# Performance work log

Measured on AMD Instinct MI355X. Metric: run time of the kernel, lower is better.

The kernel has to match this reference:

```python
import jax, jax.numpy as jnp
import numpy as np

B, T, D = 8, 8192, 512
H, P = 4, 24
HD = D // H
TEMP = 0.07
TOPK = max(1, int(P * 0.5))  # 12
LN_EPS = 1e-5
NORM_EPS = 1e-12


def setup_inputs() -> dict:
    key = jax.random.key(0)
    ks = jax.random.split(key, 12)
    s = 0.02
    return {
        "x": jax.random.normal(ks[0], (B, T, D), dtype=jnp.float32),
        "proto": jax.random.normal(ks[1], (P, D), dtype=jnp.float32) * s,
        "ln_g": jnp.ones((D,), dtype=jnp.float32),
        "ln_b": jnp.zeros((D,), dtype=jnp.float32),
        "Wq": jax.random.normal(ks[2], (D, D), dtype=jnp.float32) * s,
        "Wk": jax.random.normal(ks[3], (D, D), dtype=jnp.float32) * s,
        "Wv": jax.random.normal(ks[4], (D, D), dtype=jnp.float32) * s,
        "W1": jax.random.normal(ks[5], (D, D), dtype=jnp.float32) * s,
        "b1": jnp.zeros((D,), dtype=jnp.float32),
        "W2": jax.random.normal(ks[6], (D, D), dtype=jnp.float32) * s,
        "b2": jnp.zeros((D,), dtype=jnp.float32),
    }


def _l2norm(t):
    n = jnp.sqrt(jnp.sum(t * t, axis=-1, keepdims=True))
    return t / jnp.maximum(n, NORM_EPS)


def reference(x, proto, ln_g, ln_b, Wq, Wk, Wv, W1, b1, W2, b2):
    # pre-LayerNorm over last dim
    mu = jnp.mean(x, axis=-1, keepdims=True)
    var = jnp.mean((x - mu) ** 2, axis=-1, keepdims=True)
    xn = (x - mu) / jnp.sqrt(var + LN_EPS) * ln_g + ln_b

    K = xn @ Wk.T                      # [B,T,D]
    V = xn @ Wv.T                      # [B,T,D]
    Qp = proto @ Wq.T                  # [P,D] (shared across batch)

    Qh = _l2norm(Qp.reshape(P, H, HD).transpose(1, 0, 2))          # [H,P,hd]
    Kh = _l2norm(K.reshape(B, T, H, HD).transpose(0, 2, 1, 3))      # [B,H,T,hd]
    Vh = V.reshape(B, T, H, HD).transpose(0, 2, 1, 3)               # [B,H,T,hd]

    scores = jnp.einsum('hpd,bhtd->bhpt', Qh, Kh) / TEMP            # [B,H,P,T]
    attn = jnp.nan_to_num(jax.nn.softmax(scores, axis=-1), nan=0.0)
    proto_tokens = jnp.einsum('bhpt,bhtd->bhpd', attn, Vh)          # [B,H,P,hd]
    proto_tokens = proto_tokens.transpose(0, 2, 1, 3).reshape(B, P, D)

    proto_scores = jnp.sum(proto_tokens ** 2, axis=2)               # [B,P]
    _, idx = jax.lax.top_k(proto_scores, TOPK)                      # [B,topk]
    topk_tokens = jnp.take_along_axis(proto_tokens, idx[:, :, None], axis=1)
    z = jnp.mean(topk_tokens, axis=1)                               # [B,D]

    h = jax.nn.silu(z @ W1.T + b1)
    return h @ W2.T + b2
```

## Files before the change

kernel.cpp:

```cpp
#include <hip/hip_runtime.h>
#include <hip/hip_bf16.h>

#define BB 8
#define TSEQ 8192
#define DDIM 512
#define NH 4
#define HDIM 128
#define NP 24
#define NPAD 32
#define NTOPK 12
#define NCHUNK 32
#define TCHUNK 256
#define NTILES 8

typedef _Float16 half8_t __attribute__((ext_vector_type(8)));
typedef _Float16 half4_t __attribute__((ext_vector_type(4)));
typedef _Float16 half2_t __attribute__((ext_vector_type(2)));
typedef float f32x4_t __attribute__((ext_vector_type(4)));

#define MFMA(a, b, c) __builtin_amdgcn_mfma_f32_16x16x32_f16((a), (b), (c), 0, 0, 0)

#define WGBAR() do { asm volatile("s_waitcnt lgkmcnt(0)" ::: "memory"); \
                     __builtin_amdgcn_s_barrier(); } while (0)


__global__ __launch_bounds__(256) void qh_kernel(
    const float* __restrict__ proto, const float* __restrict__ Wq, float* __restrict__ qhs)
{
  const int p = blockIdx.x, tid = threadIdx.x;
  __shared__ float prow[DDIM];
  __shared__ float qp[DDIM];
  __shared__ float np[NH][8];
  __shared__ float nb[NH];
  prow[tid] = proto[(size_t)p * DDIM + tid];
  prow[tid + 256] = proto[(size_t)p * DDIM + tid + 256];
  __syncthreads();
#pragma unroll
  for (int i = 0; i < 2; ++i) {
    int dd = tid + i * 256;
    const float4* w4 = reinterpret_cast<const float4*>(Wq + (size_t)dd * DDIM);
    const float4* p4 = reinterpret_cast<const float4*>(prow);
    float s = 0.f;
    for (int d = 0; d < 128; ++d) {
      float4 av = p4[d], bv = w4[d];
      s += av.x * bv.x + av.y * bv.y + av.z * bv.z + av.w * bv.w;
    }
    qp[dd] = s;
  }
  __syncthreads();
  {
    int hh = tid >> 3, pr = tid & 7;
    if (hh < NH) {
      float s = 0.f;
      for (int k = 0; k < 16; ++k) { float v = qp[hh * HDIM + pr * 16 + k]; s += v * v; }
      np[hh][pr] = s;
    }
  }
  __syncthreads();
  if (tid < NH) {
    float s = 0.f;
    for (int k = 0; k < 8; ++k) s += np[tid][k];
    nb[tid] = 1.f / (fmaxf(sqrtf(s), 1e-12f) * 0.07f);
  }
  __syncthreads();
#pragma unroll
  for (int i = 0; i < 2; ++i) {
    int dd = tid + i * 256;
    int hh = dd >> 7, jj = dd & 127;
    qhs[((size_t)hh * NP + p) * HDIM + jj] = qp[dd] * nb[hh];
  }
}

__global__ __launch_bounds__(256) void wg16_kernel(
    const float* __restrict__ Wk, const float* __restrict__ ln_g, const float* __restrict__ ln_b,
    _Float16* __restrict__ wg16, float* __restrict__ uvK, float* __restrict__ vvK)
{
  const int j = blockIdx.x, tid = threadIdx.x;
  __shared__ float su[256], sv[256];
  float w0 = Wk[(size_t)j * 512 + tid], w1 = Wk[(size_t)j * 512 + tid + 256];
  float g0 = ln_g[tid], g1 = ln_g[tid + 256];
  float b0 = ln_b[tid], b1 = ln_b[tid + 256];
  wg16[(size_t)j * 512 + tid] = (_Float16)(w0 * g0);
  wg16[(size_t)j * 512 + tid + 256] = (_Float16)(w1 * g1);
  su[tid] = w0 * g0 + w1 * g1;
  sv[tid] = w0 * b0 + w1 * b1;
  __syncthreads();
  for (int s = 128; s > 0; s >>= 1) {
    if (tid < s) { su[tid] += su[tid + s]; sv[tid] += sv[tid + s]; }
    __syncthreads();
  }
  if (tid == 0) { uvK[j] = su[0]; vvK[j] = sv[0]; }
}

__global__ __launch_bounds__(256) void wqkg_kernel(
    const float* __restrict__ qhs, const float* __restrict__ Wk,
    const float* __restrict__ ln_g, const float* __restrict__ ln_b,
    _Float16* __restrict__ wqkg16, float* __restrict__ uq, float* __restrict__ vq)
{
  const int blk = blockIdx.x, tid = threadIdx.x;
  const int p = blk & 31, h = blk >> 5;
  __shared__ float su[256], sv[256];
  if (p >= NP) {
    wqkg16[((size_t)(h * 32 + p)) * 512 + tid] = (_Float16)0.f;
    wqkg16[((size_t)(h * 32 + p)) * 512 + tid + 256] = (_Float16)0.f;
    if (tid == 0) { uq[h * 32 + p] = 0.f; vq[h * 32 + p] = 0.f; }
    return;
  }
  __shared__ float qv[HDIM];
  if (tid < HDIM) qv[tid] = qhs[((size_t)h * NP + p) * HDIM + tid];
  __syncthreads();
  float s0 = 0.f, s1 = 0.f;
  for (int j = 0; j < HDIM; ++j) {
    float q = qv[j];
    const float* wr = Wk + (size_t)(h * 128 + j) * 512;
    s0 += q * wr[tid];
    s1 += q * wr[tid + 256];
  }
  float g0 = ln_g[tid], g1 = ln_g[tid + 256];
  float b0 = ln_b[tid], b1 = ln_b[tid + 256];
  wqkg16[((size_t)(h * 32 + p)) * 512 + tid] = (_Float16)(s0 * g0);
  wqkg16[((size_t)(h * 32 + p)) * 512 + tid + 256] = (_Float16)(s1 * g1);
  su[tid] = s0 * g0 + s1 * g1;
  sv[tid] = s0 * b0 + s1 * b1;
  __syncthreads();
  for (int s = 128; s > 0; s >>= 1) {
    if (tid < s) { su[tid] += su[tid + s]; sv[tid] += sv[tid + s]; }
    __syncthreads();
  }
  if (tid == 0) { uq[h * 32 + p] = su[0]; vq[h * 32 + p] = sv[0]; }
}

__global__ __launch_bounds__(512, 1) void knorm6(
    const float* __restrict__ x, const _Float16* __restrict__ wg16,
    const float* __restrict__ uvK, const float* __restrict__ vvK,
    float* __restrict__ normINV, float* __restrict__ miv)
{
  const int tid = threadIdx.x;
  const int w = tid >> 6, l = tid & 63;
  const int g = l >> 4, a = l & 15;
  const int blk = blockIdx.x;
  const int tc = blk & 31, g2 = (blk >> 5) & 1, b = blk >> 6;
  const int ct0 = tc * 256;

  __shared__ __align__(16) unsigned char xs_raw[32 * 1040];
  __shared__ float normp_s[8][32];
  __shared__ float2 miv_s[32];

  const int jrow0 = g2 * 256 + 32 * w + a;
  half8_t wgf[2][16];
#pragma unroll
  for (int kst = 0; kst < 16; ++kst) {
    wgf[0][kst] = *reinterpret_cast<const half8_t*>(wg16 + (size_t)jrow0 * 512 + kst * 32 + g * 8);
    wgf[1][kst] = *reinterpret_cast<const half8_t*>(wg16 + (size_t)(jrow0 + 16) * 512 + kst * 32 + g * 8);
  }
  const float u0 = uvK[jrow0], u1 = uvK[jrow0 + 16];
  const float v0 = vvK[jrow0], v1 = vvK[jrow0 + 16];

  const float4* xc4 = reinterpret_cast<const float4*>(x) + ((size_t)(b * TSEQ + ct0)) * 128;

  float4 praw[4][2];
#pragma unroll
  for (int tt = 0; tt < 4; ++tt)
#pragma unroll
    for (int i = 0; i < 2; ++i)
      praw[tt][i] = xc4[(size_t)(4 * w + tt) * 128 + l + 64 * i];

  for (int tile = 0; tile < NTILES; ++tile) {
    float sA[4], sB[4];
#pragma unroll
    for (int tt = 0; tt < 4; ++tt) {
      float4 v0f = praw[tt][0], v1f = praw[tt][1];
      sA[tt] = (v0f.x + v0f.y) + (v0f.z + v0f.w) + (v1f.x + v1f.y) + (v1f.z + v1f.w);
      sB[tt] = (v0f.x * v0f.x + v0f.y * v0f.y) + (v0f.z * v0f.z + v0f.w * v0f.w)
             + (v1f.x * v1f.x + v1f.y * v1f.y) + (v1f.z * v1f.z + v1f.w * v1f.w);
    }
#pragma unroll
    for (int m = 1; m < 64; m <<= 1)
#pragma unroll
      for (int tt = 0; tt < 4; ++tt) { sA[tt] += __shfl_xor(sA[tt], m); sB[tt] += __shfl_xor(sB[tt], m); }
    float muv[4], ivv[4];
#pragma unroll
    for (int tt = 0; tt < 4; ++tt) {
      float mu = sA[tt] * (1.f / 512.f);
      float var = sB[tt] * (1.f / 512.f) - mu * mu;
      muv[tt] = mu; ivv[tt] = rsqrtf(var + 1e-5f);
    }

    WGBAR();

#pragma unroll
    for (int tt = 0; tt < 4; ++tt)
#pragma unroll
      for (int i = 0; i < 2; ++i) {
        float4 v = praw[tt][i];
        half4_t hx;
        hx[0] = (_Float16)v.x; hx[1] = (_Float16)v.y; hx[2] = (_Float16)v.z; hx[3] = (_Float16)v.w;
        *reinterpret_cast<half4_t*>(xs_raw + (4 * w + tt) * 1040 + 8 * l + 512 * i) = hx;
      }
#pragma unroll
    for (int tt = 0; tt < 4; ++tt) {
      if (l == tt) {
        miv_s[4 * w + tt] = make_float2(muv[tt], ivv[tt]);
        if (g2 == 0) {
          size_t t = (size_t)b * TSEQ + ct0 + tile * 32 + 4 * w + tt;
          miv[2 * t] = muv[tt];
          miv[2 * t + 1] = ivv[tt];
        }
      }
    }
    if (tile + 1 < NTILES) {
#pragma unroll
      for (int tt = 0; tt < 4; ++tt)
#pragma unroll
        for (int i = 0; i < 2; ++i)
          praw[tt][i] = xc4[(size_t)((tile + 1) * 32 + 4 * w + tt) * 128 + l + 64 * i];
    }
    WGBAR();

    f32x4_t kacc[2][2];
    const f32x4_t vzero = {0.f, 0.f, 0.f, 0.f};
    kacc[0][0] = vzero; kacc[0][1] = vzero; kacc[1][0] = vzero; kacc[1][1] = vzero;
#pragma unroll
    for (int kst = 0; kst < 16; ++kst) {
#pragma unroll
      for (int mt = 0; mt < 2; ++mt) {
        half8_t af = *reinterpret_cast<const half8_t*>(xs_raw + (16 * mt + a) * 1040 + kst * 64 + g * 16);
        kacc[mt][0] = MFMA(af, wgf[0][kst], kacc[mt][0]);
        kacc[mt][1] = MFMA(af, wgf[1][kst], kacc[mt][1]);
      }
    }
    float np2[2][4];
#pragma unroll
    for (int mt = 0; mt < 2; ++mt)
#pragma unroll
      for (int r = 0; r < 4; ++r) {
        float2 mvt = miv_s[16 * mt + 4 * g + r];
        float k0 = mvt.y * (kacc[mt][0][r] - mvt.x * u0) + v0;
        float k1 = mvt.y * (kacc[mt][1][r] - mvt.x * u1) + v1;
        np2[mt][r] = k0 * k0 + k1 * k1;
      }
#pragma unroll
    for (int m = 1; m < 16; m <<= 1)
#pragma unroll
      for (int mt = 0; mt < 2; ++mt)
#pragma unroll
        for (int r = 0; r < 4; ++r) np2[mt][r] += __shfl_xor(np2[mt][r], m);
    if (a == 0) {
#pragma unroll
      for (int mt = 0; mt < 2; ++mt)
#pragma unroll
        for (int r = 0; r < 4; ++r) normp_s[w][16 * mt + 4 * g + r] = np2[mt][r];
    }
    WGBAR();
    if (tid < 64) {
      const int t = tid & 31, hl = tid >> 5;
      float s = normp_s[hl * 4 + 0][t] + normp_s[hl * 4 + 1][t]
              + normp_s[hl * 4 + 2][t] + normp_s[hl * 4 + 3][t];
      normINV[((size_t)b * NH + 2 * g2 + hl) * TSEQ + ct0 + tile * 32 + t] =
          rsqrtf(fmaxf(s, 1e-24f));
    }
  }
}

__global__ __launch_bounds__(512, 1) void attn6(
    const float* __restrict__ x, const _Float16* __restrict__ wqkg16,
    const float* __restrict__ normINV, const float* __restrict__ miv,
    const float* __restrict__ uq, const float* __restrict__ vq,
    const float* __restrict__ ln_g, const float* __restrict__ ln_b,
    float* __restrict__ ml, _Float16* __restrict__ xbar)
{
  const int tid = threadIdx.x;
  const int w = tid >> 6, l = tid & 63;
  const int g = l >> 4, a = l & 15;
  const int blk = blockIdx.x;
  const int c = blk & 31, g2 = (blk >> 5) & 1, b = blk >> 6;

  __shared__ __align__(16) unsigned char xs_raw[32 * 1040];
  __shared__ __align__(16) unsigned char xt_raw[512 * 72];
  __shared__ __align__(16) unsigned char wl_raw[64 * 80];
  __shared__ float mArr_s[64], lArr_s[64], fbuf_s[64], c1Arr_s[64];

  if (tid < 64) { mArr_s[tid] = -1e30f; lArr_s[tid] = 0.f; c1Arr_s[tid] = 0.f; }

  f32x4_t acc3[4][4];
  const f32x4_t vzero = {0.f, 0.f, 0.f, 0.f};
#pragma unroll
  for (int mA = 0; mA < 4; ++mA)
#pragma unroll
    for (int nt = 0; nt < 4; ++nt) acc3[mA][nt] = vzero;

  const float4* xc4 = reinterpret_cast<const float4*>(x) + ((size_t)(b * TSEQ + c * TCHUNK)) * 128;
  const _Float16* wqbase = wqkg16 + ((size_t)(g2 * 64 + 16 * w + a)) * 512 + g * 8;
  const float* nbase0 = normINV + ((size_t)b * NH + 2 * g2 + (w >> 1)) * TSEQ + c * TCHUNK;
  const float* mivc = miv + 2 * ((size_t)b * TSEQ + c * TCHUNK);
  float uqp = 0.f, vqp = 0.f;
  if (w < 4) { uqp = uq[g2 * 64 + 16 * w + a]; vqp = vq[g2 * 64 + 16 * w + a]; }

  float4 praw[4][2];
#pragma unroll
  for (int tt = 0; tt < 4; ++tt)
#pragma unroll
    for (int i = 0; i < 2; ++i)
      praw[tt][i] = xc4[(size_t)(4 * w + tt) * 128 + l + 64 * i];

  for (int tile = 0; tile < NTILES; ++tile) {
    WGBAR();

#pragma unroll
    for (int tt = 0; tt < 4; ++tt)
#pragma unroll
      for (int i = 0; i < 2; ++i) {
        float4 v = praw[tt][i];
        half4_t hx;
        hx[0] = (_Float16)v.x; hx[1] = (_Float16)v.y; hx[2] = (_Float16)v.z; hx[3] = (_Float16)v.w;
        *reinterpret_cast<half4_t*>(xs_raw + (4 * w + tt) * 1040 + 8 * l + 512 * i) = hx;
      }
    {
      const float* pf = reinterpret_cast<const float*>(praw);
#pragma unroll
      for (int i = 0; i < 2; ++i)
#pragma unroll
        for (int e = 0; e < 4; ++e) {
          half4_t hv;
          hv[0] = (_Float16)pf[0 * 8 + i * 4 + e];
          hv[1] = (_Float16)pf[1 * 8 + i * 4 + e];
          hv[2] = (_Float16)pf[2 * 8 + i * 4 + e];
          hv[3] = (_Float16)pf[3 * 8 + i * 4 + e];
          int d = 4 * l + 256 * i + e;
          *reinterpret_cast<half4_t*>(xt_raw + d * 72 + 8 * (w ^ ((d >> 4) & 7))) = hv;
        }
    }
    if (tile + 1 < NTILES) {
#pragma unroll
      for (int tt = 0; tt < 4; ++tt)
#pragma unroll
        for (int i = 0; i < 2; ++i)
          praw[tt][i] = xc4[(size_t)((tile + 1) * 32 + 4 * w + tt) * 128 + l + 64 * i];
    }
    f32x4_t niv4[2];
    f32x4_t mv[2][2];
    if (w < 4) {
      const float* nb2 = nbase0 + tile * 32 + 4 * g;
      niv4[0] = *reinterpret_cast<const f32x4_t*>(nb2);
      niv4[1] = *reinterpret_cast<const f32x4_t*>(nb2 + 16);
#pragma unroll
      for (int mt = 0; mt < 2; ++mt) {
        const float* mb = mivc + 2 * (tile * 32 + 16 * mt + 4 * g);
        mv[mt][0] = *reinterpret_cast<const f32x4_t*>(mb);
        mv[mt][1] = *reinterpret_cast<const f32x4_t*>(mb + 4);
      }
    }
    WGBAR();

    if (w < 4) {
      f32x4_t qacc[2] = {vzero, vzero};
#pragma unroll
      for (int kst = 0; kst < 16; ++kst) {
        half8_t bq8 = *reinterpret_cast<const half8_t*>(wqbase + kst * 32);
#pragma unroll
        for (int mt = 0; mt < 2; ++mt) {
          half8_t af = *reinterpret_cast<const half8_t*>(xs_raw + (16 * mt + a) * 1040 + kst * 64 + g * 16);
          qacc[mt] = MFMA(af, bq8, qacc[mt]);
        }
      }
      const int p = 16 * w + a;
      float sc[2][4], ivr[2][4], imr[2][4];
      float cmax = -3e38f;
#pragma unroll
      for (int mt = 0; mt < 2; ++mt)
#pragma unroll
        for (int r = 0; r < 4; ++r) {
          float mu = mv[mt][r >> 1][2 * (r & 1)];
          float iv = mv[mt][r >> 1][2 * (r & 1) + 1];
          ivr[mt][r] = iv;
          imr[mt][r] = iv * mu;
          float s = (iv * (qacc[mt][r] - mu * uqp) + vqp) * niv4[mt][r];
          sc[mt][r] = s;
          cmax = fmaxf(cmax, s);
        }
      cmax = fmaxf(cmax, __shfl_xor(cmax, 16));
      cmax = fmaxf(cmax, __shfl_xor(cmax, 32));
      float mo = mArr_s[p];
      float mn = fmaxf(mo, cmax);
      float fe = __expf(mo - mn);
      float ls = 0.f, ls1 = 0.f;
#pragma unroll
      for (int mt = 0; mt < 2; ++mt) {
        half4_t wp;
#pragma unroll
        for (int r = 0; r < 4; ++r) {
          float e = __expf(sc[mt][r] - mn);
          ls += e;
          ls1 += e * imr[mt][r];
          wp[r] = (_Float16)(e * ivr[mt][r]);
        }
        *reinterpret_cast<half4_t*>(wl_raw + p * 80 + 32 * mt + 8 * g) = wp;
      }
      ls += __shfl_xor(ls, 16);   ls += __shfl_xor(ls, 32);
      ls1 += __shfl_xor(ls1, 16); ls1 += __shfl_xor(ls1, 32);
      if (l < 16) {
        mArr_s[p] = mn;
        lArr_s[p] = lArr_s[p] * fe + ls;
        c1Arr_s[p] = c1Arr_s[p] * fe + ls1;
        fbuf_s[p] = fe;
      }
    }
    WGBAR();

#pragma unroll
    for (int mA = 0; mA < 4; ++mA)
#pragma unroll
      for (int r = 0; r < 4; ++r) {
        float f = fbuf_s[16 * mA + 4 * g + r];
#pragma unroll
        for (int nt = 0; nt < 4; ++nt) acc3[mA][nt][r] *= f;
      }
    {
      half8_t wlf[4];
#pragma unroll
      for (int mA = 0; mA < 4; ++mA)
        wlf[mA] = *reinterpret_cast<const half8_t*>(wl_raw + (16 * mA + a) * 80 + 16 * g);
#pragma unroll
      for (int nt = 0; nt < 4; ++nt) {
        const int d = 64 * w + 16 * nt + a;
        const unsigned char* rowp = xt_raw + d * 72;
        const int key = (d >> 4) & 7;
        half4_t lo = *reinterpret_cast<const half4_t*>(rowp + 8 * ((2 * g) ^ key));
        half4_t hi = *reinterpret_cast<const half4_t*>(rowp + 8 * ((2 * g + 1) ^ key));
        half8_t bf;
        bf[0] = lo[0]; bf[1] = lo[1]; bf[2] = lo[2]; bf[3] = lo[3];
        bf[4] = hi[0]; bf[5] = hi[1]; bf[6] = hi[2]; bf[7] = hi[3];
#pragma unroll
        for (int mA = 0; mA < 4; ++mA) acc3[mA][nt] = MFMA(wlf[mA], bf, acc3[mA][nt]);
      }
    }
  }

  __syncthreads();
  float gd[4], bd[4];
#pragma unroll
  for (int nt = 0; nt < 4; ++nt) {
    gd[nt] = ln_g[64 * w + 16 * nt + a];
    bd[nt] = ln_b[64 * w + 16 * nt + a];
  }
#pragma unroll
  for (int mA = 0; mA < 4; ++mA)
#pragma unroll
    for (int r = 0; r < 4; ++r) {
      const int p = 16 * mA + 4 * g + r;
      const float c1p = c1Arr_s[p], lp = lArr_s[p];
      const int h = 2 * g2 + (p >> 5), ph = p & 31;
      _Float16* xb = xbar + ((((size_t)b * NH + h) * NCHUNK + c) * NPAD + ph) * DDIM;
#pragma unroll
      for (int nt = 0; nt < 4; ++nt)
        xb[64 * w + 16 * nt + a] = (_Float16)(gd[nt] * (acc3[mA][nt][r] - c1p) + bd[nt] * lp);
    }
  if (tid < 64) {
    const int h = 2 * g2 + (tid >> 5), ph = tid & 31;
    size_t mlb = ((((size_t)b * NH + h) * NCHUNK + c) * NPAD + ph) * 2;
    ml[mlb] = mArr_s[tid];
    ml[mlb + 1] = lArr_s[tid];
  }
}

__global__ __launch_bounds__(256) void reduce_proto(
    const float* __restrict__ ml, const _Float16* __restrict__ xbar,
    const float* __restrict__ Wv, float* __restrict__ proto_t)
{
  const int tid = threadIdx.x;
  const int blk = blockIdx.x;
  const int p = blk % NP;
  const int h = (blk / NP) % NH;
  const int b = blk / (NP * NH);
  const int wv = tid >> 6, ln = tid & 63;

  __shared__ float fch[NCHUNK];
  __shared__ float LinvS;
  __shared__ __align__(16) float xbs[DDIM];

  if (tid < NCHUNK) {
    size_t idx = ((((size_t)b * NH + h) * NCHUNK + tid) * NPAD + p) * 2;
    float m = ml[idx], lv = ml[idx + 1];
    float mstar = m;
#pragma unroll
    for (int k = 16; k >= 1; k >>= 1) mstar = fmaxf(mstar, __shfl_xor(mstar, k));
    float f = __expf(m - mstar);
    float Lp = lv * f;
#pragma unroll
    for (int k = 16; k >= 1; k >>= 1) Lp += __shfl_xor(Lp, k);
    fch[tid] = f;
    if (tid == 0) LinvS = 1.f / fmaxf(Lp, 1e-30f);
  }
  __syncthreads();
  float a0 = 0.f, a1 = 0.f;
  for (int cc = 0; cc < NCHUNK; ++cc) {
    float f = fch[cc];
    const _Float16* src = xbar + ((((size_t)b * NH + h) * NCHUNK + cc) * NPAD + p) * DDIM;
    half2_t v = *reinterpret_cast<const half2_t*>(src + 2 * tid);
    a0 += f * (float)v[0];
    a1 += f * (float)v[1];
  }
  xbs[2 * tid] = a0;
  xbs[2 * tid + 1] = a1;
  __syncthreads();
  const float Linv = LinvS;
  const float4* zp = reinterpret_cast<const float4*>(xbs);
  const float4 z0 = zp[2 * ln], z1 = zp[2 * ln + 1];
#pragma unroll 4
  for (int j0 = 0; j0 < 32; ++j0) {
    const int j = wv * 32 + j0;
    const float4* wrow = reinterpret_cast<const float4*>(Wv + (size_t)(h * HDIM + j) * DDIM);
    float4 w0 = wrow[2 * ln], w1 = wrow[2 * ln + 1];
    float s = w0.x * z0.x + w0.y * z0.y + w0.z * z0.z + w0.w * z0.w
            + w1.x * z1.x + w1.y * z1.y + w1.z * z1.z + w1.w * z1.w;
#pragma unroll
    for (int m = 1; m < 64; m <<= 1) s += __shfl_xor(s, m);
    if (ln == 0)
      proto_t[((size_t)b * NP + p) * DDIM + h * HDIM + j] = s * Linv;
  }
}

__global__ __launch_bounds__(256) void topk_mean(
    const float* __restrict__ proto_t, float* __restrict__ zbuf)
{
  const int b = blockIdx.x, tid = threadIdx.x;
  __shared__ float pt[NP][DDIM];
  __shared__ float spart[NP][8];
  __shared__ float sc[NP];
  __shared__ int sel[NP];
  for (int i = tid; i < NP * DDIM; i += 256) pt[i >> 9][i & 511] = proto_t[(size_t)b * NP * DDIM + i];
  __syncthreads();
  {
    int p = tid >> 3, pr = tid & 7;
    if (p < NP) {
      float s = 0.f;
      for (int k = 0; k < 64; ++k) { float v = pt[p][pr * 64 + k]; s += v * v; }
      spart[p][pr] = s;
    }
  }
  __syncthreads();
  if (tid < NP) {
    float s = 0.f;
    for (int k = 0; k < 8; ++k) s += spart[tid][k];
    sc[tid] = s;
  }
  __syncthreads();
  if (tid < NP) {
    float sv = sc[tid]; int rank = 0;
    for (int q = 0; q < NP; ++q) { float so = sc[q]; if (so > sv || (so == sv && q < tid)) ++rank; }
    sel[tid] = (rank < NTOPK) ? 1 : 0;
  }
  __syncthreads();
#pragma unroll
  for (int i = 0; i < 2; ++i) {
    const int d = tid + i * 256;
    float z0 = 0.f;
#pragma unroll
    for (int p = 0; p < NP; ++p)
      if (sel[p]) z0 += pt[p][d];
    zbuf[(size_t)b * DDIM + d] = z0 * (1.f / NTOPK);
  }
}

template <int ACT>
__global__ __launch_bounds__(256) void mlp_fc(
    const float* __restrict__ zin, const float* __restrict__ W,
    const float* __restrict__ bias, float* __restrict__ outp)
{
  const int tid = threadIdx.x;
  const int wv = tid >> 6, ln = tid & 63;
  const int j = blockIdx.x * 4 + wv;
  __shared__ __align__(16) float zs[BB][DDIM];
  for (int i = tid; i < BB * DDIM; i += 256) zs[i >> 9][i & 511] = zin[i];
  __syncthreads();
  const float4* wrow = reinterpret_cast<const float4*>(W + (size_t)j * DDIM);
  const float4 w0 = wrow[2 * ln], w1 = wrow[2 * ln + 1];
  const float bj = bias[j];
#pragma unroll
  for (int b = 0; b < BB; ++b) {
    const float4* zp = reinterpret_cast<const float4*>(zs[b]);
    float4 z0 = zp[2 * ln], z1 = zp[2 * ln + 1];
    float s = w0.x * z0.x + w0.y * z0.y + w0.z * z0.z + w0.w * z0.w
            + w1.x * z1.x + w1.y * z1.y + w1.z * z1.z + w1.w * z1.w;
#pragma unroll
    for (int m = 1; m < 64; m <<= 1) s += __shfl_xor(s, m);
    if (ln == b) {
      s += bj;
      if (ACT) s = s / (1.f + expf(-s));
      outp[(size_t)b * DDIM + j] = s;
    }
  }
}

extern "C" void kernel_launch(void* const* d_in, const int* in_sizes, int n_in,
                              void* d_out, int out_size, void* d_ws, size_t ws_size,
                              hipStream_t stream)
{
  const float* x    = (const float*)d_in[0];
  const float* prt  = (const float*)d_in[1];
  const float* ln_g = (const float*)d_in[2];
  const float* ln_b = (const float*)d_in[3];
  const float* Wq   = (const float*)d_in[4];
  const float* Wk   = (const float*)d_in[5];
  const float* Wv   = (const float*)d_in[6];
  const float* W1   = (const float*)d_in[7];
  const float* b1   = (const float*)d_in[8];
  const float* W2   = (const float*)d_in[9];
  const float* b2   = (const float*)d_in[10];
  float* out = (float*)d_out;
  float* ws = (float*)d_ws;

  float* qhs = ws;
  float* ml  = ws + 12288;
  _Float16* xb16 = (_Float16*)(ws + 77824);
  float* pt  = ws + 8466432;
  _Float16* wg16   = (_Float16*)(ws + 8564736);
  _Float16* wqkg16 = (_Float16*)(ws + 8695808);
  float* normINV = ws + 8728576;
  float* miv     = ws + 8990720;
  float* uvK     = ws + 9121792;
  float* vvK     = ws + 9122304;
  float* uq      = ws + 9122816;
  float* vq      = ws + 9122944;
  float* zbuf    = ws + 9123072;
  float* hbuf    = ws + 9127168;

  qh_kernel<<<NP, 256, 0, stream>>>(prt, Wq, qhs);
  wg16_kernel<<<512, 256, 0, stream>>>(Wk, ln_g, ln_b, wg16, uvK, vvK);
  wqkg_kernel<<<128, 256, 0, stream>>>(qhs, Wk, ln_g, ln_b, wqkg16, uq, vq);
  knorm6<<<BB * 2 * 32, 512, 0, stream>>>(x, wg16, uvK, vvK, normINV, miv);
  attn6<<<BB * 2 * NCHUNK, 512, 0, stream>>>(x, wqkg16, normINV, miv, uq, vq, ln_g, ln_b, ml, xb16);
  reduce_proto<<<BB * NH * NP, 256, 0, stream>>>(ml, xb16, Wv, pt);
  topk_mean<<<BB, 256, 0, stream>>>(pt, zbuf);
  mlp_fc<1><<<128, 256, 0, stream>>>(zbuf, W1, b1, hbuf);
  mlp_fc<0><<<128, 256, 0, stream>>>(hbuf, W2, b2, out);
}
```

Before: 241.4 us.

## Fuse key-norm computation into attention kernel using idle warps

```diff
diff --git a/kernel.cpp b/kernel.cpp
--- a/kernel.cpp
+++ b/kernel.cpp
@@ -130,33 +130,49 @@
   if (tid == 0) { uq[h * 32 + p] = su[0]; vq[h * 32 + p] = sv[0]; }
 }
 
-__global__ __launch_bounds__(512, 1) void knorm6(
+__global__ __launch_bounds__(512, 1) void attn7(
     const float* __restrict__ x, const _Float16* __restrict__ wg16,
+    const _Float16* __restrict__ wqkg16,
     const float* __restrict__ uvK, const float* __restrict__ vvK,
-    float* __restrict__ normINV, float* __restrict__ miv)
+    const float* __restrict__ uq, const float* __restrict__ vq,
+    const float* __restrict__ ln_g, const float* __restrict__ ln_b,
+    float* __restrict__ ml, _Float16* __restrict__ xbar)
 {
   const int tid = threadIdx.x;
   const int w = tid >> 6, l = tid & 63;
   const int g = l >> 4, a = l & 15;
   const int blk = blockIdx.x;
-  const int tc = blk & 31, g2 = (blk >> 5) & 1, b = blk >> 6;
-  const int ct0 = tc * 256;
+  const int c = blk & 31, g2 = (blk >> 5) & 1, b = blk >> 6;
 
   __shared__ __align__(16) unsigned char xs_raw[32 * 1040];
-  __shared__ float normp_s[8][32];
+  __shared__ __align__(16) unsigned char xt_raw[512 * 72];
+  __shared__ __align__(16) unsigned char wl_raw[64 * 80];
+  __shared__ float mArr_s[64], lArr_s[64], fbuf_s[64], c1Arr_s[64];
+  __shared__ float normp_s[4][32];
   __shared__ float2 miv_s[32];
 
-  const int jrow0 = g2 * 256 + 32 * w + a;
-  half8_t wgf[2][16];
-#pragma unroll
-  for (int kst = 0; kst < 16; ++kst) {
-    wgf[0][kst] = *reinterpret_cast<const half8_t*>(wg16 + (size_t)jrow0 * 512 + kst * 32 + g * 8);
-    wgf[1][kst] = *reinterpret_cast<const half8_t*>(wg16 + (size_t)(jrow0 + 16) * 512 + kst * 32 + g * 8);
-  }
-  const float u0 = uvK[jrow0], u1 = uvK[jrow0 + 16];
-  const float v0 = vvK[jrow0], v1 = vvK[jrow0 + 16];
-
-  const float4* xc4 = reinterpret_cast<const float4*>(x) + ((size_t)(b * TSEQ + ct0)) * 128;
+  if (tid < 64) { mArr_s[tid] = -1e30f; lArr_s[tid] = 0.f; c1Arr_s[tid] = 0.f; }
+
+  f32x4_t acc3[4][4];
+  const f32x4_t vzero = {0.f, 0.f, 0.f, 0.f};
+#pragma unroll
+  for (int mA = 0; mA < 4; ++mA)
+#pragma unroll
+    for (int nt = 0; nt < 4; ++nt) acc3[mA][nt] = vzero;
+
+  const float4* xc4 = reinterpret_cast<const float4*>(x) + ((size_t)(b * TSEQ + c * TCHUNK)) * 128;
+  const _Float16* wqbase = wqkg16 + ((size_t)(g2 * 64 + 16 * w + a)) * 512 + g * 8;
+  const int q = w & 3;
+  const int jrow0 = g2 * 256 + 64 * q + a;
+  float uqp = 0.f, vqp = 0.f;
+  float uK[4], vK[4];
+  if (w < 4) {
+    uqp = uq[g2 * 64 + 16 * w + a];
+    vqp = vq[g2 * 64 + 16 * w + a];
+  } else {
+#pragma unroll
+    for (int nt = 0; nt < 4; ++nt) { uK[nt] = uvK[jrow0 + 16 * nt]; vK[nt] = vvK[jrow0 + 16 * nt]; }
+  }
 
   float4 praw[4][2];
 #pragma unroll
@@ -186,124 +202,6 @@
       muv[tt] = mu; ivv[tt] = rsqrtf(var + 1e-5f);
     }
 
-    WGBAR();
-
-#pragma unroll
-    for (int tt = 0; tt < 4; ++tt)
-#pragma unroll
-      for (int i = 0; i < 2; ++i) {
-        float4 v = praw[tt][i];
-        half4_t hx;
-        hx[0] = (_Float16)v.x; hx[1] = (_Float16)v.y; hx[2] = (_Float16)v.z; hx[3] = (_Float16)v.w;
-        *reinterpret_cast<half4_t*>(xs_raw + (4 * w + tt) * 1040 + 8 * l + 512 * i) = hx;
-      }
-#pragma unroll
-    for (int tt = 0; tt < 4; ++tt) {
-      if (l == tt) {
-        miv_s[4 * w + tt] = make_float2(muv[tt], ivv[tt]);
-        if (g2 == 0) {
-          size_t t = (size_t)b * TSEQ + ct0 + tile * 32 + 4 * w + tt;
-          miv[2 * t] = muv[tt];
-          miv[2 * t + 1] = ivv[tt];
-        }
-      }
-    }
-    if (tile + 1 < NTILES) {
-#pragma unroll
-      for (int tt = 0; tt < 4; ++tt)
-#pragma unroll
-        for (int i = 0; i < 2; ++i)
-          praw[tt][i] = xc4[(size_t)((tile + 1) * 32 + 4 * w + tt) * 128 + l + 64 * i];
-    }
-    WGBAR();
-
-    f32x4_t kacc[2][2];
-    const f32x4_t vzero = {0.f, 0.f, 0.f, 0.f};
-    kacc[0][0] = vzero; kacc[0][1] = vzero; kacc[1][0] = vzero; kacc[1][1] = vzero;
-#pragma unroll
-    for (int kst = 0; kst < 16; ++kst) {
-#pragma unroll
-      for (int mt = 0; mt < 2; ++mt) {
-        half8_t af = *reinterpret_cast<const half8_t*>(xs_raw + (16 * mt + a) * 1040 + kst * 64 + g * 16);
-        kacc[mt][0] = MFMA(af, wgf[0][kst], kacc[mt][0]);
-        kacc[mt][1] = MFMA(af, wgf[1][kst], kacc[mt][1]);
-      }
-    }
-    float np2[2][4];
-#pragma unroll
-    for (int mt = 0; mt < 2; ++mt)
-#pragma unroll
-      for (int r = 0; r < 4; ++r) {
-        float2 mvt = miv_s[16 * mt + 4 * g + r];
-        float k0 = mvt.y * (kacc[mt][0][r] - mvt.x * u0) + v0;
-        float k1 = mvt.y * (kacc[mt][1][r] - mvt.x * u1) + v1;
-        np2[mt][r] = k0 * k0 + k1 * k1;
-      }
-#pragma unroll
-    for (int m = 1; m < 16; m <<= 1)
-#pragma unroll
-      for (int mt = 0; mt < 2; ++mt)
-#pragma unroll
-        for (int r = 0; r < 4; ++r) np2[mt][r] += __shfl_xor(np2[mt][r], m);
-    if (a == 0) {
-#pragma unroll
-      for (int mt = 0; mt < 2; ++mt)
-#pragma unroll
-        for (int r = 0; r < 4; ++r) normp_s[w][16 * mt + 4 * g + r] = np2[mt][r];
-    }
-    WGBAR();
-    if (tid < 64) {
-      const int t = tid & 31, hl = tid >> 5;
-      float s = normp_s[hl * 4 + 0][t] + normp_s[hl * 4 + 1][t]
-              + normp_s[hl * 4 + 2][t] + normp_s[hl * 4 + 3][t];
-      normINV[((size_t)b * NH + 2 * g2 + hl) * TSEQ + ct0 + tile * 32 + t] =
-          rsqrtf(fmaxf(s, 1e-24f));
-    }
-  }
-}
-
-__global__ __launch_bounds__(512, 1) void attn6(
-    const float* __restrict__ x, const _Float16* __restrict__ wqkg16,
-    const float* __restrict__ normINV, const float* __restrict__ miv,
-    const float* __restrict__ uq, const float* __restrict__ vq,
-    const float* __restrict__ ln_g, const float* __restrict__ ln_b,
-    float* __restrict__ ml, _Float16* __restrict__ xbar)
-{
-  const int tid = threadIdx.x;
-  const int w = tid >> 6, l = tid & 63;
-  const int g = l >> 4, a = l & 15;
-  const int blk = blockIdx.x;
-  const int c = blk & 31, g2 = (blk >> 5) & 1, b = blk >> 6;
-
-  __shared__ __align__(16) unsigned char xs_raw[32 * 1040];
-  __shared__ __align__(16) unsigned char xt_raw[512 * 72];
-  __shared__ __align__(16) unsigned char wl_raw[64 * 80];
-  __shared__ float mArr_s[64], lArr_s[64], fbuf_s[64], c1Arr_s[64];
-
-  if (tid < 64) { mArr_s[tid] = -1e30f; lArr_s[tid] = 0.f; c1Arr_s[tid] = 0.f; }
-
-  f32x4_t acc3[4][4];
-  const f32x4_t vzero = {0.f, 0.f, 0.f, 0.f};
-#pragma unroll
-  for (int mA = 0; mA < 4; ++mA)
-#pragma unroll
-    for (int nt = 0; nt < 4; ++nt) acc3[mA][nt] = vzero;
-
-  const float4* xc4 = reinterpret_cast<const float4*>(x) + ((size_t)(b * TSEQ + c * TCHUNK)) * 128;
-  const _Float16* wqbase = wqkg16 + ((size_t)(g2 * 64 + 16 * w + a)) * 512 + g * 8;
-  const float* nbase0 = normINV + ((size_t)b * NH + 2 * g2 + (w >> 1)) * TSEQ + c * TCHUNK;
-  const float* mivc = miv + 2 * ((size_t)b * TSEQ + c * TCHUNK);
-  float uqp = 0.f, vqp = 0.f;
-  if (w < 4) { uqp = uq[g2 * 64 + 16 * w + a]; vqp = vq[g2 * 64 + 16 * w + a]; }
-
-  float4 praw[4][2];
-#pragma unroll
-  for (int tt = 0; tt < 4; ++tt)
-#pragma unroll
-    for (int i = 0; i < 2; ++i)
-      praw[tt][i] = xc4[(size_t)(4 * w + tt) * 128 + l + 64 * i];
-
-  for (int tile = 0; tile < NTILES; ++tile) {
     WGBAR();
 
 #pragma unroll
@@ -330,6 +228,9 @@
           *reinterpret_cast<half4_t*>(xt_raw + d * 72 + 8 * (w ^ ((d >> 4) & 7))) = hv;
         }
     }
+#pragma unroll
+    for (int tt = 0; tt < 4; ++tt)
+      if (l == tt) miv_s[4 * w + tt] = make_float2(muv[tt], ivv[tt]);
     if (tile + 1 < NTILES) {
 #pragma unroll
       for (int tt = 0; tt < 4; ++tt)
@@ -337,23 +238,10 @@
         for (int i = 0; i < 2; ++i)
           praw[tt][i] = xc4[(size_t)((tile + 1) * 32 + 4 * w + tt) * 128 + l + 64 * i];
     }
-    f32x4_t niv4[2];
-    f32x4_t mv[2][2];
+    WGBAR();
+
+    f32x4_t qacc[2] = {vzero, vzero};
     if (w < 4) {
-      const float* nb2 = nbase0 + tile * 32 + 4 * g;
-      niv4[0] = *reinterpret_cast<const f32x4_t*>(nb2);
-      niv4[1] = *reinterpret_cast<const f32x4_t*>(nb2 + 16);
-#pragma unroll
-      for (int mt = 0; mt < 2; ++mt) {
-        const float* mb = mivc + 2 * (tile * 32 + 16 * mt + 4 * g);
-        mv[mt][0] = *reinterpret_cast<const f32x4_t*>(mb);
-        mv[mt][1] = *reinterpret_cast<const f32x4_t*>(mb + 4);
-      }
-    }
-    WGBAR();
-
-    if (w < 4) {
-      f32x4_t qacc[2] = {vzero, vzero};
 #pragma unroll
       for (int kst = 0; kst < 16; ++kst) {
         half8_t bq8 = *reinterpret_cast<const half8_t*>(wqbase + kst * 32);
@@ -363,6 +251,57 @@
           qacc[mt] = MFMA(af, bq8, qacc[mt]);
         }
       }
+    } else {
+      f32x4_t kacc[2][4];
+#pragma unroll
+      for (int mt = 0; mt < 2; ++mt)
+#pragma unroll
+        for (int nt = 0; nt < 4; ++nt) kacc[mt][nt] = vzero;
+#pragma unroll
+      for (int kst = 0; kst < 16; ++kst) {
+        half8_t bnt[4];
+#pragma unroll
+        for (int nt = 0; nt < 4; ++nt)
+          bnt[nt] = *reinterpret_cast<const half8_t*>(
+              wg16 + (size_t)(jrow0 + 16 * nt) * 512 + kst * 32 + g * 8);
+#pragma unroll
+        for (int mt = 0; mt < 2; ++mt) {
+          half8_t af = *reinterpret_cast<const half8_t*>(xs_raw + (16 * mt + a) * 1040 + kst * 64 + g * 16);
+#pragma unroll
+          for (int nt = 0; nt < 4; ++nt) kacc[mt][nt] = MFMA(af, bnt[nt], kacc[mt][nt]);
+        }
+      }
+      float np2[2][4];
+#pragma unroll
+      for (int mt = 0; mt < 2; ++mt)
+#pragma unroll
+        for (int r = 0; r < 4; ++r) {
+          float2 mvt = miv_s[16 * mt + 4 * g + r];
+          float s = 0.f;
+#pragma unroll
+          for (int nt = 0; nt < 4; ++nt) {
+            float k = mvt.y * (kacc[mt][nt][r] - mvt.x * uK[nt]) + vK[nt];
+            s += k * k;
+          }
+          np2[mt][r] = s;
+        }
+#pragma unroll
+      for (int m = 1; m < 16; m <<= 1)
+#pragma unroll
+        for (int mt = 0; mt < 2; ++mt)
+#pragma unroll
+          for (int r = 0; r < 4; ++r) np2[mt][r] += __shfl_xor(np2[mt][r], m);
+      if (a == 0) {
+#pragma unroll
+        for (int mt = 0; mt < 2; ++mt)
+#pragma unroll
+          for (int r = 0; r < 4; ++r) normp_s[q][16 * mt + 4 * g + r] = np2[mt][r];
+      }
+    }
+    WGBAR();
+
+    if (w < 4) {
+      const int hl = w >> 1;
       const int p = 16 * w + a;
       float sc[2][4], ivr[2][4], imr[2][4];
       float cmax = -3e38f;
@@ -370,11 +309,13 @@
       for (int mt = 0; mt < 2; ++mt)
 #pragma unroll
         for (int r = 0; r < 4; ++r) {
-          float mu = mv[mt][r >> 1][2 * (r & 1)];
-          float iv = mv[mt][r >> 1][2 * (r & 1) + 1];
-          ivr[mt][r] = iv;
-          imr[mt][r] = iv * mu;
-          float s = (iv * (qacc[mt][r] - mu * uqp) + vqp) * niv4[mt][r];
+          const int t = 16 * mt + 4 * g + r;
+          float2 mvt = miv_s[t];
+          float n2 = normp_s[2 * hl][t] + normp_s[2 * hl + 1][t];
+          float niv = rsqrtf(fmaxf(n2, 1e-24f));
+          ivr[mt][r] = mvt.y;
+          imr[mt][r] = mvt.y * mvt.x;
+          float s = (mvt.y * (qacc[mt][r] - mvt.x * uqp) + vqp) * niv;
           sc[mt][r] = s;
           cmax = fmaxf(cmax, s);
         }
@@ -616,8 +557,6 @@
   float* pt  = ws + 8466432;
   _Float16* wg16   = (_Float16*)(ws + 8564736);
   _Float16* wqkg16 = (_Float16*)(ws + 8695808);
-  float* normINV = ws + 8728576;
-  float* miv     = ws + 8990720;
   float* uvK     = ws + 9121792;
   float* vvK     = ws + 9122304;
   float* uq      = ws + 9122816;
@@ -628,8 +567,8 @@
   qh_kernel<<<NP, 256, 0, stream>>>(prt, Wq, qhs);
   wg16_kernel<<<512, 256, 0, stream>>>(Wk, ln_g, ln_b, wg16, uvK, vvK);
   wqkg_kernel<<<128, 256, 0, stream>>>(qhs, Wk, ln_g, ln_b, wqkg16, uq, vq);
-  knorm6<<<BB * 2 * 32, 512, 0, stream>>>(x, wg16, uvK, vvK, normINV, miv);
-  attn6<<<BB * 2 * NCHUNK, 512, 0, stream>>>(x, wqkg16, normINV, miv, uq, vq, ln_g, ln_b, ml, xb16);
+  attn7<<<BB * 2 * NCHUNK, 512, 0, stream>>>(x, wg16, wqkg16, uvK, vvK, uq, vq,
+                                             ln_g, ln_b, ml, xb16);
   reduce_proto<<<BB * NH * NP, 256, 0, stream>>>(ml, xb16, Wv, pt);
   topk_mean<<<BB, 256, 0, stream>>>(pt, zbuf);
   mlp_fc<1><<<128, 256, 0, stream>>>(zbuf, W1, b1, hbuf);
```

After: 355.6 us. +47.3%, slower.
